# Kernel optimization log

Hardware: AMD Instinct MI355X
Metric: run time of the kernel (lower is better)

The kernel has to match this reference:

```python
import jax, jax.numpy as jnp
import numpy as np

B, S, D, H = 2048, 200, 128, 4
H1, H2 = 64, 32
F = 4 * D
TIME_DECAY = 0.1


def setup_inputs() -> dict:
    key = jax.random.key(0)
    ks = jax.random.split(key, 10)
    query = jax.random.normal(ks[0], (B, D), dtype=jnp.float32)
    keys = jax.random.normal(ks[1], (B, S, D), dtype=jnp.float32)
    keys_mask = jax.random.randint(ks[2], (B, S), 0, 2).astype(bool)
    keys_mask = keys_mask.at[:, 0].set(True)  # avoid fully-masked rows
    sc = 0.02
    # per-head MLP params, stacked over heads
    W1 = sc * jax.random.normal(ks[3], (H, H1, F), dtype=jnp.float32)
    b1 = jnp.zeros((H, H1), dtype=jnp.float32)
    a1 = 0.25 * jnp.ones((H,), dtype=jnp.float32)  # PReLU (default single param)
    W2 = sc * jax.random.normal(ks[4], (H, H2, H1), dtype=jnp.float32)
    b2 = jnp.zeros((H, H2), dtype=jnp.float32)
    a2 = 0.25 * jnp.ones((H,), dtype=jnp.float32)
    W3 = sc * jax.random.normal(ks[5], (H, H2), dtype=jnp.float32)
    b3 = jnp.zeros((H,), dtype=jnp.float32)
    Wo = sc * jax.random.normal(ks[6], (D, D), dtype=jnp.float32)
    bo = jnp.zeros((D,), dtype=jnp.float32)
    return {"query": query, "keys": keys, "keys_mask": keys_mask,
            "W1": W1, "b1": b1, "a1": a1, "W2": W2, "b2": b2, "a2": a2,
            "W3": W3, "b3": b3, "Wo": Wo, "bo": bo}


def reference(query, keys, keys_mask, W1, b1, a1, W2, b2, a2, W3, b3, Wo, bo):
    b, s, d = keys.shape
    q = query[:, None, :]                                    # [B,1,D]
    x = jnp.concatenate(
        [keys, jnp.broadcast_to(q, (b, s, d)), keys * q, keys - q], axis=-1)  # [B,S,4D]
    pos = jnp.arange(s, dtype=keys.dtype)
    tw = jnp.exp(TIME_DECAY * (pos - s + 1))                 # [S]
    # all heads batched: [B,H,S,H1]
    h = jnp.einsum('bsf,hdf->bhsd', x, W1) + b1[None, :, None, :]
    h = jnp.where(h >= 0, h, a1[None, :, None, None] * h)    # PReLU
    h = jnp.einsum('bhsd,hed->bhse', h, W2) + b2[None, :, None, :]
    h = jnp.where(h >= 0, h, a2[None, :, None, None] * h)
    scores = jnp.einsum('bhse,he->bhs', h, W3) + b3[None, :, None]
    scores = scores * tw[None, None, :]
    scores = jnp.where(keys_mask[:, None, :], scores, -1e9)
    w = jax.nn.softmax(scores, axis=-1)                      # [B,H,S]
    out_h = jnp.einsum('bhs,bsd->bhd', w, keys)              # [B,H,D]
    combined = out_h.mean(axis=1)                            # [B,D]
    output = combined @ Wo.T + bo                            # [B,D]
    avg_weights = w.mean(axis=1)                             # [B,S]
    return output, avg_weights
```

## Files before the change

### kernel.cpp

```cpp
#include <hip/hip_runtime.h>
#include <hip/hip_bf16.h>
#include <stdint.h>

#define Bsz 2048
#define Ssz 200
#define Dsz 128
#define Hsz 4
#define SP  224

typedef __attribute__((ext_vector_type(8))) short short8;
typedef __attribute__((ext_vector_type(4))) float f32x4;
typedef unsigned short ushort_t;
typedef unsigned int uint_t;

#define KEYS_OFF   0
#define W1EFF_OFF  57344
#define H1C_OFF    122880
#define W2S_OFF    139264
#define SCW_OFF    155648
#define C1S_OFF    159232
#define QS_OFF     160256
#define B2S_OFF    160768
#define W3S_OFF    161280
#define MASK_OFF   161792
#define COMB_OFF   162688
#define A1S_OFF    163200
#define A2S_OFF    163216
#define B3S_OFF    163232
#define SMEM_BYTES 163248

__device__ __forceinline__ ushort_t f2bf(float x) {
    union { float f; uint_t u; } v; v.f = x;
    uint_t u = v.u;
    u += 0x7FFFu + ((u >> 16) & 1u);
    return (ushort_t)(u >> 16);
}

__global__ void prep_kernel(const float* __restrict__ W1, const float* __restrict__ W2,
                            const float* __restrict__ Wo,
                            float* __restrict__ W1sum, float* __restrict__ W1c,
                            float* __restrict__ W1diffT, float* __restrict__ WoT,
                            ushort_t* __restrict__ W2bf) {
    int i = blockIdx.x * blockDim.x + threadIdx.x;
    if (i < 32768) {
        int n = i >> 7, j = i & 127;
        float a  = W1[n * 512 + j];
        float dd = W1[n * 512 + 384 + j];
        W1sum[i] = a + dd;
        W1c[i]   = W1[n * 512 + 256 + j];
        W1diffT[j * 256 + n] = W1[n * 512 + 128 + j] - dd;
    }
    if (i < 16384) {
        int j = i >> 7, d = i & 127;
        WoT[i] = Wo[d * 128 + j];
    }
    if (i < 8192) W2bf[i] = f2bf(W2[i]);
}

__global__ void c1_kernel(const float* __restrict__ query, const float* __restrict__ W1diffT,
                          const float* __restrict__ b1, float* __restrict__ c1out) {
    __shared__ float qs[128];
    int b = blockIdx.x, t = threadIdx.x;
    if (t < 128) qs[t] = query[b * 128 + t];
    __syncthreads();
    float acc = b1[t];
    #pragma unroll 8
    for (int j = 0; j < 128; ++j) acc += W1diffT[j * 256 + t] * qs[j];
    c1out[b * 256 + t] = acc;
}

__launch_bounds__(512, 2)
__global__ void attn_kernel(const float* __restrict__ query, const float* __restrict__ keys,
                            const int* __restrict__ kmask,
                            const float* __restrict__ a1, const float* __restrict__ b2,
                            const float* __restrict__ a2, const float* __restrict__ W3,
                            const float* __restrict__ b3, const float* __restrict__ bo,
                            const float* __restrict__ W1sum, const float* __restrict__ W1c,
                            const float* __restrict__ WoT, const ushort_t* __restrict__ W2bf,
                            const float* __restrict__ c1ws, float* __restrict__ out) {
    extern __shared__ char smem[];
    const int tid = threadIdx.x;
    const int bb  = blockIdx.x;
    const int w   = tid >> 6;
    const int l   = tid & 63;
    const int l15 = l & 15;
    const int lk  = l >> 4;

    float* qs   = (float*)(smem + QS_OFF);
    float* b2s  = (float*)(smem + B2S_OFF);
    float* w3s  = (float*)(smem + W3S_OFF);
    float* c1s  = (float*)(smem + C1S_OFF);
    float* scw  = (float*)(smem + SCW_OFF);
    int*   mks  = (int*)(smem + MASK_OFF);
    float* comb = (float*)(smem + COMB_OFF);
    float* a1s  = (float*)(smem + A1S_OFF);
    float* a2s  = (float*)(smem + A2S_OFF);
    float* b3s  = (float*)(smem + B3S_OFF);

    if (tid < 128) qs[tid] = query[bb * 128 + tid];
    else if (tid < 256) b2s[tid - 128] = b2[tid - 128];
    else if (tid < 384) w3s[tid - 256] = W3[tid - 256];
    else if (tid < 396) {
        int i = tid - 384;
        if (i < 4) a1s[i] = a1[i];
        else if (i < 8) a2s[i - 4] = a2[i - 4];
        else b3s[i - 8] = b3[i - 8];
    }
    if (tid < SP)  mks[tid] = (tid < Ssz) ? kmask[bb * Ssz + tid] : 0;
    if (tid < 256) c1s[tid] = c1ws[bb * 256 + tid];
    __syncthreads();

    #pragma unroll
    for (int it = 0; it < 14; ++it) {
        int id = tid + 512 * it;
        int row = id >> 5, c4 = id & 31;
        float4 kv = {0.f, 0.f, 0.f, 0.f};
        if (row < Ssz) kv = *(const float4*)(keys + (size_t)(bb * Ssz + row) * Dsz + c4 * 4);
        uint_t p0 = (uint_t)f2bf(kv.x) | ((uint_t)f2bf(kv.y) << 16);
        uint_t p1 = (uint_t)f2bf(kv.z) | ((uint_t)f2bf(kv.w) << 16);
        int off = KEYS_OFF + (((row << 8) + (c4 << 3)) ^ ((row & 7) << 4));
        *(uint_t*)(smem + off)     = p0;
        *(uint_t*)(smem + off + 4) = p1;
    }
    const uint_t* W2u = (const uint_t*)W2bf;
    #pragma unroll
    for (int it = 0; it < 8; ++it) {
        int p = tid + 512 * it;
        int flat = p * 2;
        int h = flat >> 11, rem = flat & 2047;
        int e = rem >> 6, k = rem & 63;
        int off = W2S_OFF + ((((h << 12) + (e << 7) + (k << 1))) ^ ((e & 7) << 4));
        *(uint_t*)(smem + off) = W2u[p];
    }
    const float2* Ws2 = (const float2*)W1sum;
    const float2* Wc2 = (const float2*)W1c;
    #pragma unroll
    for (int it = 0; it < 32; ++it) {
        int p = tid + 512 * it;
        int n = p >> 6, jp = p & 63;
        float2 sv = Ws2[p];
        float2 cv = Wc2[p];
        float q0 = qs[jp * 2], q1 = qs[jp * 2 + 1];
        uint_t pk = (uint_t)f2bf(sv.x + cv.x * q0) | ((uint_t)f2bf(sv.y + cv.y * q1) << 16);
        int off = W1EFF_OFF + ((((n << 8) + (jp << 2))) ^ ((n & 7) << 4));
        *(uint_t*)(smem + off) = pk;
    }
    __syncthreads();

    const int wr = w >> 2;
    const int wc = w & 3;
    const f32x4 fz = {0.f, 0.f, 0.f, 0.f};
    f32x4 acc[7][4];
    #pragma unroll
    for (int m = 0; m < 7; ++m)
        #pragma unroll
        for (int n = 0; n < 4; ++n) acc[m][n] = fz;

    #pragma unroll
    for (int t = 0; t < 4; ++t) {
        short8 bfr[4];
        #pragma unroll
        for (int nt = 0; nt < 4; ++nt) {
            int n = wc * 64 + nt * 16 + l15;
            int off = W1EFF_OFF + ((((n << 8) + (t * 64 + lk * 16))) ^ ((n & 7) << 4));
            bfr[nt] = *(const short8*)(smem + off);
        }
        #pragma unroll
        for (int mt = 0; mt < 7; ++mt) {
            int gmt = wr * 7 + mt;
            if (gmt < 13) {
                int row = gmt * 16 + l15;
                int off = KEYS_OFF + ((((row << 8) + (t * 64 + lk * 16))) ^ ((row & 7) << 4));
                short8 afr = *(const short8*)(smem + off);
                #pragma unroll
                for (int nt = 0; nt < 4; ++nt)
                    acc[mt][nt] = __builtin_amdgcn_mfma_f32_16x16x32_bf16(afr, bfr[nt], acc[mt][nt], 0, 0, 0);
            }
        }
    }

    float c1v[4];
    #pragma unroll
    for (int nt = 0; nt < 4; ++nt) c1v[nt] = c1s[wc * 64 + nt * 16 + l15];
    const float a1v = a1s[wc];
    const int h2  = w >> 1;
    const int mtl = w & 1;
    float b2v[2], w3v[2];
    #pragma unroll
    for (int nt = 0; nt < 2; ++nt) {
        b2v[nt] = b2s[h2 * 32 + nt * 16 + l15];
        w3v[nt] = w3s[h2 * 32 + nt * 16 + l15];
    }
    const float a2v = a2s[h2];
    const float b3v = b3s[h2];

    for (int c = 0; c < 7; ++c) {
        #pragma unroll
        for (int mt = 0; mt < 7; ++mt) {
            int gmt = wr * 7 + mt;
            if (gmt < 13 && (gmt == 2 * c || gmt == 2 * c + 1)) {
                int rbase = (gmt - 2 * c) * 16 + lk * 4;
                #pragma unroll
                for (int nt = 0; nt < 4; ++nt) {
                    int n = wc * 64 + nt * 16 + l15;
                    #pragma unroll
                    for (int r = 0; r < 4; ++r) {
                        float v = acc[mt][nt][r] + c1v[nt];
                        v = (v >= 0.f) ? v : a1v * v;
                        int lrow = rbase + r;
                        int off = H1C_OFF + ((((lrow << 9) + (n << 1))) ^ ((lrow & 7) << 4));
                        *(ushort_t*)(smem + off) = f2bf(v);
                    }
                }
            }
        }
        __syncthreads();
        if (c < 6 || mtl == 0) {
            f32x4 acc2[2];
            acc2[0] = fz; acc2[1] = fz;
            #pragma unroll
            for (int kt = 0; kt < 2; ++kt) {
                int lrow = mtl * 16 + l15;
                int k = kt * 32 + lk * 8;
                int aoff = H1C_OFF + ((((lrow << 9) + ((h2 * 64 + k) << 1))) ^ ((lrow & 7) << 4));
                short8 afr = *(const short8*)(smem + aoff);
                #pragma unroll
                for (int nt = 0; nt < 2; ++nt) {
                    int e = nt * 16 + l15;
                    int boff = W2S_OFF + ((((h2 << 12) + (e << 7) + (k << 1))) ^ ((e & 7) << 4));
                    short8 bfr2 = *(const short8*)(smem + boff);
                    acc2[nt] = __builtin_amdgcn_mfma_f32_16x16x32_bf16(afr, bfr2, acc2[nt], 0, 0, 0);
                }
            }
            #pragma unroll
            for (int r = 0; r < 4; ++r) {
                float sum = 0.f;
                #pragma unroll
                for (int nt = 0; nt < 2; ++nt) {
                    float v = acc2[nt][r] + b2v[nt];
                    v = (v >= 0.f) ? v : a2v * v;
                    sum += v * w3v[nt];
                }
                sum += __shfl_xor(sum, 1);
                sum += __shfl_xor(sum, 2);
                sum += __shfl_xor(sum, 4);
                sum += __shfl_xor(sum, 8);
                if (l15 == 0) {
                    int sg = 32 * c + mtl * 16 + lk * 4 + r;
                    float tw = __expf(0.1f * (float)(sg - (Ssz - 1)));
                    float sc = (sum + b3v) * tw;
                    scw[h2 * SP + sg] = mks[sg] ? sc : -1.0e9f;
                }
            }
        }
        __syncthreads();
    }

    if (w < 4) {
        float xv[4], ex[4];
        float mx = -3.0e38f;
        #pragma unroll
        for (int i = 0; i < 4; ++i) {
            int s = l + 64 * i;
            xv[i] = (s < Ssz) ? scw[w * SP + s] : -1.0e30f;
            mx = fmaxf(mx, xv[i]);
        }
        #pragma unroll
        for (int m = 1; m < 64; m <<= 1) mx = fmaxf(mx, __shfl_xor(mx, m));
        float sm = 0.f;
        #pragma unroll
        for (int i = 0; i < 4; ++i) {
            int s = l + 64 * i;
            ex[i] = (s < Ssz) ? __expf(xv[i] - mx) : 0.f;
            sm += ex[i];
        }
        #pragma unroll
        for (int m = 1; m < 64; m <<= 1) sm += __shfl_xor(sm, m);
        float inv = 1.0f / sm;
        #pragma unroll
        for (int i = 0; i < 4; ++i) {
            int s = l + 64 * i;
            if (s < SP) scw[w * SP + s] = ex[i] * inv;
        }
    }
    __syncthreads();

    if (tid < Ssz) {
        float aw = 0.25f * (scw[tid] + scw[SP + tid] + scw[2 * SP + tid] + scw[3 * SP + tid]);
        out[Bsz * Dsz + bb * Ssz + tid] = aw;
    }

    f32x4 acc4 = fz;
    #pragma unroll
    for (int t = 0; t < 7; ++t) {
        int k0 = t * 32 + lk * 8;
        short8 afr = {0, 0, 0, 0, 0, 0, 0, 0};
        if (l15 < 4) {
            const float* wp = scw + l15 * SP + k0;
            #pragma unroll
            for (int j = 0; j < 8; ++j) afr[j] = (short)f2bf(wp[j]);
        }
        short8 bfr;
        #pragma unroll
        for (int j = 0; j < 8; ++j) {
            int srow = k0 + j;
            int off = KEYS_OFF + ((((srow << 8) + ((16 * w + l15) << 1))) ^ ((srow & 7) << 4));
            bfr[j] = *(const short*)(smem + off);
        }
        acc4 = __builtin_amdgcn_mfma_f32_16x16x32_bf16(afr, bfr, acc4, 0, 0, 0);
    }
    if (lk == 0) comb[16 * w + l15] = 0.25f * (acc4[0] + acc4[1] + acc4[2] + acc4[3]);
    __syncthreads();

    if (tid < Dsz) {
        float o = bo[tid];
        #pragma unroll 8
        for (int j = 0; j < Dsz; ++j) o += comb[j] * WoT[j * Dsz + tid];
        out[bb * Dsz + tid] = o;
    }
}

extern "C" void kernel_launch(void* const* d_in, const int* in_sizes, int n_in,
                              void* d_out, int out_size, void* d_ws, size_t ws_size,
                              hipStream_t stream) {
    const float* query = (const float*)d_in[0];
    const float* keys  = (const float*)d_in[1];
    const int*   kmask = (const int*)d_in[2];
    const float* W1    = (const float*)d_in[3];
    const float* b1    = (const float*)d_in[4];
    const float* a1    = (const float*)d_in[5];
    const float* W2    = (const float*)d_in[6];
    const float* b2    = (const float*)d_in[7];
    const float* a2    = (const float*)d_in[8];
    const float* W3    = (const float*)d_in[9];
    const float* b3    = (const float*)d_in[10];
    const float* Wo    = (const float*)d_in[11];
    const float* bo    = (const float*)d_in[12];
    float* out = (float*)d_out;

    char* ws = (char*)d_ws;
    float*    W1sum   = (float*)(ws);
    float*    W1c     = (float*)(ws + 131072);
    float*    W1diffT = (float*)(ws + 262144);
    float*    WoT     = (float*)(ws + 393216);
    ushort_t* W2bf    = (ushort_t*)(ws + 458752);
    float*    c1ws    = (float*)(ws + 475136);

    hipFuncSetAttribute(reinterpret_cast<const void*>(attn_kernel),
                        hipFuncAttributeMaxDynamicSharedMemorySize, SMEM_BYTES);

    prep_kernel<<<128, 256, 0, stream>>>(W1, W2, Wo, W1sum, W1c, W1diffT, WoT, W2bf);
    c1_kernel<<<Bsz, 256, 0, stream>>>(query, W1diffT, b1, c1ws);
    attn_kernel<<<Bsz, 512, SMEM_BYTES, stream>>>(query, keys, kmask, a1, b2, a2, W3, b3, bo,
                                                  W1sum, W1c, WoT, W2bf, c1ws, out);
}
```

Baseline: 261.6 us.

## Reuse W1 smem for H1, cut layer-2 barriers, prepack bf16 weights, split Wo GEMV

The H1 activation buffer now reuses the W1-effective shared-memory region after the first GEMM, which needs one extra barrier. Layer 2 then runs in two large row chunks instead of seven small ones, so far fewer block-wide barriers are needed. Softmax weights are also written once as zero-padded bf16 into shared memory, so the final MFMA loads them directly instead of converting floats per lane. The output GEMV is split across all 512 threads with a partial-sum reduction. The launch bounds change from 2 blocks to 1 block per CU, which frees registers but may lower occupancy.

```diff
diff --git a/kernel.cpp b/kernel.cpp
--- a/kernel.cpp
+++ b/kernel.cpp
@@ -7,6 +7,7 @@
 #define Dsz 128
 #define Hsz 4
 #define SP  224
+#define SPB 232
 
 typedef __attribute__((ext_vector_type(8))) short short8;
 typedef __attribute__((ext_vector_type(4))) float f32x4;
@@ -14,20 +15,21 @@
 typedef unsigned int uint_t;
 
 #define KEYS_OFF   0
-#define W1EFF_OFF  57344
-#define H1C_OFF    122880
-#define W2S_OFF    139264
-#define SCW_OFF    155648
-#define C1S_OFF    159232
-#define QS_OFF     160256
-#define B2S_OFF    160768
-#define W3S_OFF    161280
-#define MASK_OFF   161792
-#define COMB_OFF   162688
-#define A1S_OFF    163200
-#define A2S_OFF    163216
-#define B3S_OFF    163232
-#define SMEM_BYTES 163248
+#define W1H_OFF    57344
+#define W2S_OFF    122880
+#define SCW_OFF    139264
+#define SCWB_OFF   142848
+#define C1S_OFF    150272
+#define QS_OFF     151296
+#define B2S_OFF    151808
+#define W3S_OFF    152320
+#define MASK_OFF   152832
+#define COMB_OFF   153728
+#define PO_OFF     154240
+#define A1S_OFF    156288
+#define A2S_OFF    156304
+#define B3S_OFF    156320
+#define SMEM_BYTES 156336
 
 __device__ __forceinline__ ushort_t f2bf(float x) {
     union { float f; uint_t u; } v; v.f = x;
@@ -69,7 +71,7 @@
     c1out[b * 256 + t] = acc;
 }
 
-__launch_bounds__(512, 2)
+__launch_bounds__(512, 1)
 __global__ void attn_kernel(const float* __restrict__ query, const float* __restrict__ keys,
                             const int* __restrict__ kmask,
                             const float* __restrict__ a1, const float* __restrict__ b2,
@@ -93,6 +95,7 @@
     float* scw  = (float*)(smem + SCW_OFF);
     int*   mks  = (int*)(smem + MASK_OFF);
     float* comb = (float*)(smem + COMB_OFF);
+    float* po   = (float*)(smem + PO_OFF);
     float* a1s  = (float*)(smem + A1S_OFF);
     float* a2s  = (float*)(smem + A2S_OFF);
     float* b3s  = (float*)(smem + B3S_OFF);
@@ -108,6 +111,10 @@
     }
     if (tid < SP)  mks[tid] = (tid < Ssz) ? kmask[bb * Ssz + tid] : 0;
     if (tid < 256) c1s[tid] = c1ws[bb * 256 + tid];
+    {
+        uint_t* zb = (uint_t*)(smem + SCWB_OFF);
+        for (int i = tid; i < 1856; i += 512) zb[i] = 0;
+    }
     __syncthreads();
 
     #pragma unroll
@@ -142,7 +149,7 @@
         float2 cv = Wc2[p];
         float q0 = qs[jp * 2], q1 = qs[jp * 2 + 1];
         uint_t pk = (uint_t)f2bf(sv.x + cv.x * q0) | ((uint_t)f2bf(sv.y + cv.y * q1) << 16);
-        int off = W1EFF_OFF + ((((n << 8) + (jp << 2))) ^ ((n & 7) << 4));
+        int off = W1H_OFF + ((((n << 8) + (jp << 2))) ^ ((n & 7) << 4));
         *(uint_t*)(smem + off) = pk;
     }
     __syncthreads();
@@ -162,7 +169,7 @@
         #pragma unroll
         for (int nt = 0; nt < 4; ++nt) {
             int n = wc * 64 + nt * 16 + l15;
-            int off = W1EFF_OFF + ((((n << 8) + (t * 64 + lk * 16))) ^ ((n & 7) << 4));
+            int off = W1H_OFF + ((((n << 8) + (t * 64 + lk * 16))) ^ ((n & 7) << 4));
             bfr[nt] = *(const short8*)(smem + off);
         }
         #pragma unroll
@@ -178,13 +185,13 @@
             }
         }
     }
+    __syncthreads();
 
     float c1v[4];
     #pragma unroll
     for (int nt = 0; nt < 4; ++nt) c1v[nt] = c1s[wc * 64 + nt * 16 + l15];
     const float a1v = a1s[wc];
-    const int h2  = w >> 1;
-    const int mtl = w & 1;
+    const int h2 = w >> 1;
     float b2v[2], w3v[2];
     #pragma unroll
     for (int nt = 0; nt < 2; ++nt) {
@@ -194,35 +201,38 @@
     const float a2v = a2s[h2];
     const float b3v = b3s[h2];
 
-    for (int c = 0; c < 7; ++c) {
-        #pragma unroll
-        for (int mt = 0; mt < 7; ++mt) {
-            int gmt = wr * 7 + mt;
-            if (gmt < 13 && (gmt == 2 * c || gmt == 2 * c + 1)) {
-                int rbase = (gmt - 2 * c) * 16 + lk * 4;
-                #pragma unroll
-                for (int nt = 0; nt < 4; ++nt) {
-                    int n = wc * 64 + nt * 16 + l15;
+    #pragma unroll
+    for (int c = 0; c < 2; ++c) {
+        const int TT = (c == 0) ? 7 : 6;
+        if (wr == c) {
+            #pragma unroll
+            for (int mt = 0; mt < 7; ++mt) {
+                if (mt < TT) {
+                    int rbase = mt * 16 + lk * 4;
                     #pragma unroll
-                    for (int r = 0; r < 4; ++r) {
-                        float v = acc[mt][nt][r] + c1v[nt];
-                        v = (v >= 0.f) ? v : a1v * v;
-                        int lrow = rbase + r;
-                        int off = H1C_OFF + ((((lrow << 9) + (n << 1))) ^ ((lrow & 7) << 4));
-                        *(ushort_t*)(smem + off) = f2bf(v);
+                    for (int nt = 0; nt < 4; ++nt) {
+                        int n = wc * 64 + nt * 16 + l15;
+                        #pragma unroll
+                        for (int r = 0; r < 4; ++r) {
+                            float v = acc[mt][nt][r] + c1v[nt];
+                            v = (v >= 0.f) ? v : a1v * v;
+                            int lrow = rbase + r;
+                            int off = W1H_OFF + ((((lrow << 9) + (n << 1))) ^ ((lrow & 7) << 4));
+                            *(ushort_t*)(smem + off) = f2bf(v);
+                        }
                     }
                 }
             }
         }
         __syncthreads();
-        if (c < 6 || mtl == 0) {
+        for (int t2 = (w & 1); t2 < TT; t2 += 2) {
             f32x4 acc2[2];
             acc2[0] = fz; acc2[1] = fz;
             #pragma unroll
             for (int kt = 0; kt < 2; ++kt) {
-                int lrow = mtl * 16 + l15;
+                int lrow = t2 * 16 + l15;
                 int k = kt * 32 + lk * 8;
-                int aoff = H1C_OFF + ((((lrow << 9) + ((h2 * 64 + k) << 1))) ^ ((lrow & 7) << 4));
+                int aoff = W1H_OFF + ((((lrow << 9) + ((h2 * 64 + k) << 1))) ^ ((lrow & 7) << 4));
                 short8 afr = *(const short8*)(smem + aoff);
                 #pragma unroll
                 for (int nt = 0; nt < 2; ++nt) {
@@ -246,7 +256,7 @@
                 sum += __shfl_xor(sum, 4);
                 sum += __shfl_xor(sum, 8);
                 if (l15 == 0) {
-                    int sg = 32 * c + mtl * 16 + lk * 4 + r;
+                    int sg = c * 112 + t2 * 16 + lk * 4 + r;
                     float tw = __expf(0.1f * (float)(sg - (Ssz - 1)));
                     float sc = (sum + b3v) * tw;
                     scw[h2 * SP + sg] = mks[sg] ? sc : -1.0e9f;
@@ -280,7 +290,9 @@
         #pragma unroll
         for (int i = 0; i < 4; ++i) {
             int s = l + 64 * i;
-            if (s < SP) scw[w * SP + s] = ex[i] * inv;
+            float wv = ex[i] * inv;
+            if (s < SP) scw[w * SP + s] = wv;
+            if (s < SPB) *(ushort_t*)(smem + SCWB_OFF + w * (SPB * 2) + s * 2) = f2bf(wv);
         }
     }
     __syncthreads();
@@ -294,12 +306,7 @@
     #pragma unroll
     for (int t = 0; t < 7; ++t) {
         int k0 = t * 32 + lk * 8;
-        short8 afr = {0, 0, 0, 0, 0, 0, 0, 0};
-        if (l15 < 4) {
-            const float* wp = scw + l15 * SP + k0;
-            #pragma unroll
-            for (int j = 0; j < 8; ++j) afr[j] = (short)f2bf(wp[j]);
-        }
+        short8 afr = *(const short8*)(smem + SCWB_OFF + l15 * (SPB * 2) + k0 * 2);
         short8 bfr;
         #pragma unroll
         for (int j = 0; j < 8; ++j) {
@@ -312,11 +319,17 @@
     if (lk == 0) comb[16 * w + l15] = 0.25f * (acc4[0] + acc4[1] + acc4[2] + acc4[3]);
     __syncthreads();
 
+    {
+        int d = tid & 127, part = tid >> 7;
+        float o = 0.f;
+        const float* wp = WoT + (size_t)part * 32 * 128 + d;
+        #pragma unroll 8
+        for (int j = 0; j < 32; ++j) o += comb[part * 32 + j] * wp[j * 128];
+        po[part * 128 + d] = o;
+    }
+    __syncthreads();
     if (tid < Dsz) {
-        float o = bo[tid];
-        #pragma unroll 8
-        for (int j = 0; j < Dsz; ++j) o += comb[j] * WoT[j * Dsz + tid];
-        out[bb * Dsz + tid] = o;
+        out[bb * Dsz + tid] = bo[tid] + po[tid] + po[128 + tid] + po[256 + tid] + po[384 + tid];
     }
 }
 
```

Measured after the change: 225.4 us. -13.8%, faster.
